# Kernel optimization log

Measured on AMD Instinct MI355X. Metric: run time of the kernel, lower is better.

## Reference

```python
import jax, jax.numpy as jnp
import numpy as np

B, T, IN, H, OUT = 64, 512, 256, 1024, 1


def _uniform(key, shape, k):
    return jax.random.uniform(key, shape, jnp.float32, -k, k)


def setup_inputs() -> dict:
    key = jax.random.key(0)
    ks = jax.random.split(key, 12)
    k = 1.0 / np.sqrt(H)
    return {
        "x": jax.random.normal(ks[0], (B, T, IN), jnp.float32),
        "W_ih0": _uniform(ks[1], (3 * H, IN), k),
        "W_hh0": _uniform(ks[2], (3 * H, H), k),
        "b_ih0": _uniform(ks[3], (3 * H,), k),
        "b_hh0": _uniform(ks[4], (3 * H,), k),
        "W_ih1": _uniform(ks[5], (3 * H, H), k),
        "W_hh1": _uniform(ks[6], (3 * H, H), k),
        "b_ih1": _uniform(ks[7], (3 * H,), k),
        "b_hh1": _uniform(ks[8], (3 * H,), k),
        "W_fc": _uniform(ks[9], (OUT, H), 1.0 / np.sqrt(H)),
        "b_fc": _uniform(ks[10], (OUT,), 1.0 / np.sqrt(H)),
    }


def _gru_layer(x, W_ih, W_hh, b_ih, b_hh):
    # x: [B, T, D_in] -> outputs [B, T, H], final hidden [B, H]
    # Precompute input projections for all timesteps (one big GEMM).
    xg = jnp.einsum('btd,gd->btg', x, W_ih) + b_ih  # [B, T, 3H]
    xg = jnp.swapaxes(xg, 0, 1)  # [T, B, 3H]

    def step(h, xg_t):
        hg = h @ W_hh.T + b_hh  # [B, 3H]
        xr, xz, xn = jnp.split(xg_t, 3, axis=-1)
        hr, hz, hn = jnp.split(hg, 3, axis=-1)
        r = jax.nn.sigmoid(xr + hr)
        z = jax.nn.sigmoid(xz + hz)
        n = jnp.tanh(xn + r * hn)
        h_new = (1.0 - z) * n + z * h
        return h_new, h_new

    h0 = jnp.zeros((x.shape[0], W_hh.shape[1]), x.dtype)
    h_final, ys = jax.lax.scan(step, h0, xg)
    return jnp.swapaxes(ys, 0, 1), h_final


def reference(x, W_ih0, W_hh0, b_ih0, b_hh0, W_ih1, W_hh1, b_ih1, b_hh1, W_fc, b_fc):
    # Inference mode: dropout (between GRU layers and before fc) is identity.
    y0, _ = _gru_layer(x, W_ih0, W_hh0, b_ih0, b_hh0)
    _, h_last = _gru_layer(y0, W_ih1, W_hh1, b_ih1, b_hh1)
    return h_last @ W_fc.T + b_fc  # [B, OUT]
```

## Files before the change

### kernel.cpp

```cpp
#include <hip/hip_runtime.h>
#include <hip/hip_bf16.h>
#include <stdint.h>


constexpr int TSEQ = 512;
constexpr int NB   = 64;
constexpr int HD   = 1024;
constexpr int IND  = 256;
constexpr int NWG  = 256;
constexpr int FS   = 16;
constexpr int PL   = NB * HD;

typedef float f32x4  __attribute__((ext_vector_type(4)));
typedef short short8 __attribute__((ext_vector_type(8)));

__device__ __forceinline__ float bf2f(unsigned u) {
    return __builtin_bit_cast(float, u << 16);
}
__device__ __forceinline__ unsigned short f2bf(float f) {
    unsigned u = __builtin_bit_cast(unsigned, f);
    u += 0x7fffu + ((u >> 16) & 1u);
    return (unsigned short)(u >> 16);
}
__device__ __forceinline__ float sigm(float x) { return 1.0f / (1.0f + __expf(-x)); }
__device__ __forceinline__ float tanh_fast(float x) { return 1.0f - 2.0f / (1.0f + __expf(2.0f * x)); }

__device__ __forceinline__ void cstore16(unsigned short* p, unsigned short v) {
    __hip_atomic_store(p, v, __ATOMIC_RELAXED, __HIP_MEMORY_SCOPE_AGENT);
}
__device__ __forceinline__ unsigned short cload16(const unsigned short* p) {
    return __hip_atomic_load(p, __ATOMIC_RELAXED, __HIP_MEMORY_SCOPE_AGENT);
}
__device__ __forceinline__ void cstoref(float* p, float v) {
    __hip_atomic_store(p, v, __ATOMIC_RELAXED, __HIP_MEMORY_SCOPE_AGENT);
}
__device__ __forceinline__ float cloadf(const float* p) {
    return __hip_atomic_load(p, __ATOMIC_RELAXED, __HIP_MEMORY_SCOPE_AGENT);
}

#define MFMA(a, b, c) __builtin_amdgcn_mfma_f32_16x16x32_bf16((a), (b), (c), 0, 0, 0)

#define LDA16(dst, base, imm) \
    asm volatile("global_load_dwordx4 %0, %1, off offset:%2 sc0 sc1" \
                 : "=v"(dst) : "v"(base), "i"(imm))
#define LDX16(dst, base, imm) \
    asm volatile("global_load_dwordx4 %0, %1, off offset:%2" \
                 : "=v"(dst) : "v"(base), "i"(imm))
#define VWAIT(n) do { asm volatile("s_waitcnt vmcnt(" #n ")" ::: "memory"); \
                      __builtin_amdgcn_sched_barrier(0); } while (0)

__global__ void convert_w(const float* __restrict__ src, unsigned short* __restrict__ dst, int n) {
    int i = blockIdx.x * blockDim.x + threadIdx.x;
    int stride = gridDim.x * blockDim.x;
    for (; i < n; i += stride) dst[i] = f2bf(src[i]);
}

__global__ __launch_bounds__(256, 1) void gru_main(
    const float* __restrict__ x,
    const unsigned short* __restrict__ wih0,
    const unsigned short* __restrict__ whh0,
    const unsigned short* __restrict__ wih1,
    const unsigned short* __restrict__ whh1,
    const float* __restrict__ bih0, const float* __restrict__ bhh0,
    const float* __restrict__ bih1, const float* __restrict__ bhh1,
    const float* __restrict__ wfc,  const float* __restrict__ bfc,
    unsigned short* __restrict__ h0hi, unsigned short* __restrict__ h0lo,
    unsigned short* __restrict__ h1hi, unsigned short* __restrict__ h1lo,
    float* __restrict__ pbuf, int* __restrict__ pflag, int* __restrict__ arrive,
    float* __restrict__ out)
{
    const int wg    = blockIdx.x;
    const int layer = wg >> 7;
    const int kh    = (wg >> 6) & 1;
    const int cc    = wg & 63;
    const int pair  = (layer << 6) | cc;
    const int jb    = cc << 4;
    const int tid   = threadIdx.x;
    const int wid   = tid >> 6;
    const int lane  = tid & 63;
    const int l15   = lane & 15;
    const int kg8   = (lane >> 4) << 3;
    const int arow  = (wid << 4) + l15;
    const int kb    = kh << 9;
    const int kbx   = kh << 7;

    const unsigned short* Whh = layer ? whh1 : whh0;
    const unsigned short* Wih = layer ? wih1 : wih0;
    const float* bih = layer ? bih1 : bih0;
    const float* bhh = layer ? bhh1 : bhh0;
    unsigned short* hhi = layer ? h1hi : h0hi;
    unsigned short* hlo = layer ? h1lo : h0lo;

    const int jg = jb + l15;
    const int KW = layer ? HD : IND;
    const int kbi = layer ? kb : kbx;
    const unsigned short* bWR = Whh + (size_t)jg          * HD + kb + kg8;
    const unsigned short* bWZ = Whh + (size_t)(HD   + jg) * HD + kb + kg8;
    const unsigned short* bWN = Whh + (size_t)(2*HD + jg) * HD + kb + kg8;
    const unsigned short* bIR = Wih + (size_t)jg          * KW + kbi + kg8;
    const unsigned short* bIZ = Wih + (size_t)(HD   + jg) * KW + kbi + kg8;
    const unsigned short* bIN = Wih + (size_t)(2*HD + jg) * KW + kbi + kg8;

    const float bias_r  = bih[jg]        + bhh[jg];
    const float bias_z  = bih[HD + jg]   + bhh[HD + jg];
    const float bias_nx = bih[2*HD + jg];
    const float bias_nh = bhh[2*HD + jg];

    __shared__ unsigned short wlds[96 * 512];
    __shared__ float red[256];

    if (wid == 0) {
        if (layer == 0) {
            const unsigned short* gh[3] = {bWR, bWZ, bWN};
            for (int s = 0; s < 3; ++s)
                for (int b = 0; b < 16; ++b)
                    *(short8*)(wlds + (s * 16 + b) * 512 + lane * 8) =
                        *(const short8*)(gh[s] + b * 32);
            const unsigned short* gi[3] = {bIR, bIZ, bIN};
            for (int s = 0; s < 3; ++s)
                for (int b = 0; b < 4; ++b)
                    *(short8*)(wlds + (48 + s * 4 + b) * 512 + lane * 8) =
                        *(const short8*)(gi[s] + b * 32);
        } else {
            const unsigned short* g6[6] = {bWR, bWZ, bWN, bIR, bIZ, bIN};
            for (int s = 0; s < 6; ++s)
                for (int b = 0; b < 16; ++b)
                    *(short8*)(wlds + (s * 16 + b) * 512 + lane * 8) =
                        *(const short8*)(g6[s] + b * 32);
        }
    }
    __syncthreads();

#define LW(blk) (*(const short8*)(wlds + (blk) * 512 + lane * 8))

    float* pb = pbuf + (size_t)pair * (16 * 256) + (wid << 6) + lane;
    float hold[4] = {0.f, 0.f, 0.f, 0.f};

    for (int iter = 0; iter <= TSEQ; ++iter) {
        const bool active = layer ? (iter >= 1) : (iter < TSEQ);
        if (active) {
            const int t     = layer ? (iter - 1) : iter;
            const int rs    = (t + 1) & 1;
            const int wslot = t & 1;
            const unsigned short* hrhi = hhi + rs * PL;
            const unsigned short* hrlo = hlo + rs * PL;
            const unsigned short* bAh = hrhi + (size_t)arow * HD + kb + kg8;
            const unsigned short* bAl = hrlo + (size_t)arow * HD + kb + kg8;

            f32x4 ar  = {0.f, 0.f, 0.f, 0.f};
            f32x4 az  = {0.f, 0.f, 0.f, 0.f};
            f32x4 ahn = {0.f, 0.f, 0.f, 0.f};
            f32x4 axn = {0.f, 0.f, 0.f, 0.f};

            if (layer == 0) {
                const float* px = x + ((size_t)arow * TSEQ + t) * IND + kbx + kg8;
                short8 Ah[5], Al[5], Wa[3], Wb[3];
#define L0A(c) do { LDA16(Ah[(c)%5], bAh, (c)*64); LDA16(Al[(c)%5], bAl, (c)*64); } while (0)
#define L0X(c) do { LDX16(Ah[(c)%5], px, ((c)-16)*128); LDX16(Al[(c)%5], px, ((c)-16)*128+16); } while (0)
#define WPRE0(c, WB) do { \
    if ((c) < 16) { WB[0] = LW(c); WB[1] = LW(16 + (c)); WB[2] = LW(32 + (c)); } \
    else { WB[0] = LW(48 + (c) - 16); WB[1] = LW(52 + (c) - 16); WB[2] = LW(56 + (c) - 16); } } while (0)
#define MR0(c, WB) do { \
    ar  = MFMA(Ah[(c)%5], WB[0], ar);  ar  = MFMA(Al[(c)%5], WB[0], ar);  \
    az  = MFMA(Ah[(c)%5], WB[1], az);  az  = MFMA(Al[(c)%5], WB[1], az);  \
    ahn = MFMA(Ah[(c)%5], WB[2], ahn); ahn = MFMA(Al[(c)%5], WB[2], ahn); } while (0)
#define MX0(c, WB) do { \
    float4 xa = __builtin_bit_cast(float4, Ah[(c)%5]); \
    float4 xc = __builtin_bit_cast(float4, Al[(c)%5]); \
    short8 af; \
    af[0] = (short)f2bf(xa.x); af[1] = (short)f2bf(xa.y); \
    af[2] = (short)f2bf(xa.z); af[3] = (short)f2bf(xa.w); \
    af[4] = (short)f2bf(xc.x); af[5] = (short)f2bf(xc.y); \
    af[6] = (short)f2bf(xc.z); af[7] = (short)f2bf(xc.w); \
    ar  = MFMA(af, WB[0], ar); \
    az  = MFMA(af, WB[1], az); \
    axn = MFMA(af, WB[2], axn); } while (0)
                WPRE0(0, Wa);
                L0A(0); L0A(1); L0A(2); L0A(3);
                WPRE0(1,  Wb); L0A(4);  VWAIT(8); MR0(0,  Wa);
                WPRE0(2,  Wa); L0A(5);  VWAIT(8); MR0(1,  Wb);
                WPRE0(3,  Wb); L0A(6);  VWAIT(8); MR0(2,  Wa);
                WPRE0(4,  Wa); L0A(7);  VWAIT(8); MR0(3,  Wb);
                WPRE0(5,  Wb); L0A(8);  VWAIT(8); MR0(4,  Wa);
                WPRE0(6,  Wa); L0A(9);  VWAIT(8); MR0(5,  Wb);
                WPRE0(7,  Wb); L0A(10); VWAIT(8); MR0(6,  Wa);
                WPRE0(8,  Wa); L0A(11); VWAIT(8); MR0(7,  Wb);
                WPRE0(9,  Wb); L0A(12); VWAIT(8); MR0(8,  Wa);
                WPRE0(10, Wa); L0A(13); VWAIT(8); MR0(9,  Wb);
                WPRE0(11, Wb); L0A(14); VWAIT(8); MR0(10, Wa);
                WPRE0(12, Wa); L0A(15); VWAIT(8); MR0(11, Wb);
                WPRE0(13, Wb); L0X(16); VWAIT(8); MR0(12, Wa);
                WPRE0(14, Wa); L0X(17); VWAIT(8); MR0(13, Wb);
                WPRE0(15, Wb); L0X(18); VWAIT(8); MR0(14, Wa);
                WPRE0(16, Wa); L0X(19); VWAIT(8); MR0(15, Wb);
                WPRE0(17, Wb); VWAIT(6); MX0(16, Wa);
                WPRE0(18, Wa); VWAIT(4); MX0(17, Wb);
                WPRE0(19, Wb); VWAIT(2); MX0(18, Wa);
                               VWAIT(0); MX0(19, Wb);
            } else {
                const unsigned short* bAy = h0hi + (size_t)wslot * PL
                                                 + (size_t)arow * HD + kb + kg8;
                short8 Ah[5], Al[5], Ay[5], Wa[6], Wb[6];
#define L1A(c) do { LDA16(Ah[(c)%5], bAh, (c)*64); LDA16(Al[(c)%5], bAl, (c)*64); \
                    LDA16(Ay[(c)%5], bAy, (c)*64); } while (0)
#define WPRE1(c, WB) do { WB[0] = LW(c); WB[1] = LW(16 + (c)); WB[2] = LW(32 + (c)); \
    WB[3] = LW(48 + (c)); WB[4] = LW(64 + (c)); WB[5] = LW(80 + (c)); } while (0)
#define MF1(c, WB) do { \
    ar  = MFMA(Ah[(c)%5], WB[0], ar);  ar  = MFMA(Al[(c)%5], WB[0], ar);  \
    ar  = MFMA(Ay[(c)%5], WB[3], ar); \
    az  = MFMA(Ah[(c)%5], WB[1], az);  az  = MFMA(Al[(c)%5], WB[1], az);  \
    az  = MFMA(Ay[(c)%5], WB[4], az); \
    ahn = MFMA(Ah[(c)%5], WB[2], ahn); ahn = MFMA(Al[(c)%5], WB[2], ahn); \
    axn = MFMA(Ay[(c)%5], WB[5], axn); } while (0)
                WPRE1(0, Wa);
                L1A(0); L1A(1); L1A(2); L1A(3);
                WPRE1(1,  Wb); L1A(4);  VWAIT(12); MF1(0,  Wa);
                WPRE1(2,  Wa); L1A(5);  VWAIT(12); MF1(1,  Wb);
                WPRE1(3,  Wb); L1A(6);  VWAIT(12); MF1(2,  Wa);
                WPRE1(4,  Wa); L1A(7);  VWAIT(12); MF1(3,  Wb);
                WPRE1(5,  Wb); L1A(8);  VWAIT(12); MF1(4,  Wa);
                WPRE1(6,  Wa); L1A(9);  VWAIT(12); MF1(5,  Wb);
                WPRE1(7,  Wb); L1A(10); VWAIT(12); MF1(6,  Wa);
                WPRE1(8,  Wa); L1A(11); VWAIT(12); MF1(7,  Wb);
                WPRE1(9,  Wb); L1A(12); VWAIT(12); MF1(8,  Wa);
                WPRE1(10, Wa); L1A(13); VWAIT(12); MF1(9,  Wb);
                WPRE1(11, Wb); L1A(14); VWAIT(12); MF1(10, Wa);
                WPRE1(12, Wa); L1A(15); VWAIT(12); MF1(11, Wb);
                WPRE1(13, Wb); VWAIT(9); MF1(12, Wa);
                WPRE1(14, Wa); VWAIT(6); MF1(13, Wb);
                WPRE1(15, Wb); VWAIT(3); MF1(14, Wa);
                               VWAIT(0); MF1(15, Wb);
            }

            int* fp = pflag + ((size_t)iter * 128 + pair) * FS;
            if (kh) {
                #pragma unroll
                for (int e = 0; e < 4; ++e) {
                    cstoref(pb + (0 * 4 + e) * 256, ar[e]);
                    cstoref(pb + (1 * 4 + e) * 256, az[e]);
                    cstoref(pb + (2 * 4 + e) * 256, ahn[e]);
                    cstoref(pb + (3 * 4 + e) * 256, axn[e]);
                }
                asm volatile("s_waitcnt vmcnt(0)" ::: "memory");
                __hip_atomic_store(fp, 1, __ATOMIC_RELAXED, __HIP_MEMORY_SCOPE_AGENT);
            } else {
                if (tid == 0) {
                    int spins = 0;
                    while (__hip_atomic_load(fp, __ATOMIC_RELAXED,
                                             __HIP_MEMORY_SCOPE_AGENT) < 1) {
                        __builtin_amdgcn_s_sleep(1);
                        if (++spins > (1 << 20)) break;
                    }
                }
                __syncthreads();
                unsigned short* hwhi = hhi + wslot * PL;
                unsigned short* hwlo = hlo + wslot * PL;
                #pragma unroll
                for (int e = 0; e < 4; ++e) {
                    const float arr = ar[e]  + cloadf(pb + (0 * 4 + e) * 256);
                    const float azz = az[e]  + cloadf(pb + (1 * 4 + e) * 256);
                    const float ahh = ahn[e] + cloadf(pb + (2 * 4 + e) * 256);
                    const float axx = axn[e] + cloadf(pb + (3 * 4 + e) * 256);
                    const int bat = (wid << 4) + ((lane >> 4) << 2) + e;
                    const size_t idx = (size_t)bat * HD + jg;
                    float r = sigm(arr + bias_r);
                    float z = sigm(azz + bias_z);
                    float n = tanh_fast(axx + bias_nx + r * (ahh + bias_nh));
                    float hnew = (1.0f - z) * n + z * hold[e];
                    hold[e] = hnew;
                    unsigned short hi_ = f2bf(hnew);
                    cstore16(hwhi + idx, hi_);
                    cstore16(hwlo + idx, f2bf(hnew - bf2f((unsigned)hi_)));
                }
            }
        }

        asm volatile("s_waitcnt vmcnt(0)" ::: "memory");
        __syncthreads();
        if (tid == 0) {
            atomicAdd(&arrive[(size_t)iter * FS], 1);
            int spins = 0;
            while (__hip_atomic_load(&arrive[(size_t)iter * FS],
                                     __ATOMIC_RELAXED, __HIP_MEMORY_SCOPE_AGENT) < NWG) {
                __builtin_amdgcn_s_sleep(1);
                if (++spins > (1 << 20)) break;
            }
        }
        __syncthreads();
    }

    if (wg == 0) {
        const int fslot = (TSEQ - 1) & 1;
        const unsigned short* hf_hi = h1hi + (size_t)fslot * PL;
        const unsigned short* hf_lo = h1lo + (size_t)fslot * PL;
        const int bat  = tid & 63;
        const int part = tid >> 6;
        const int k0   = part * (HD / 4);
        float s = 0.0f;
        for (int k = 0; k < HD / 4; ++k) {
            size_t idx = (size_t)bat * HD + k0 + k;
            s += (bf2f((unsigned)cload16(hf_hi + idx)) +
                  bf2f((unsigned)cload16(hf_lo + idx))) * wfc[k0 + k];
        }
        red[tid] = s;
        __syncthreads();
        if (tid < 64)
            out[tid] = red[tid] + red[tid + 64] + red[tid + 128] + red[tid + 192] + bfc[0];
    }
}

extern "C" void kernel_launch(void* const* d_in, const int* in_sizes, int n_in,
                              void* d_out, int out_size, void* d_ws, size_t ws_size,
                              hipStream_t stream) {
    const float* x    = (const float*)d_in[0];
    const float* Wih0 = (const float*)d_in[1];
    const float* Whh0 = (const float*)d_in[2];
    const float* bih0 = (const float*)d_in[3];
    const float* bhh0 = (const float*)d_in[4];
    const float* Wih1 = (const float*)d_in[5];
    const float* Whh1 = (const float*)d_in[6];
    const float* bih1 = (const float*)d_in[7];
    const float* bhh1 = (const float*)d_in[8];
    const float* Wfc  = (const float*)d_in[9];
    const float* bfc  = (const float*)d_in[10];
    float* out = (float*)d_out;

    char* ws = (char*)d_ws;
    size_t off = 0;
    int* arrive = (int*)(ws + off);               off += (size_t)(TSEQ + 1) * FS * 4;
    int* pflag  = (int*)(ws + off);               off += (size_t)(TSEQ + 1) * 128 * FS * 4;
    unsigned short* h0hi = (unsigned short*)(ws + off); off += (size_t)2 * PL * 2;
    unsigned short* h0lo = (unsigned short*)(ws + off); off += (size_t)2 * PL * 2;
    unsigned short* h1hi = (unsigned short*)(ws + off); off += (size_t)2 * PL * 2;
    unsigned short* h1lo = (unsigned short*)(ws + off); off += (size_t)2 * PL * 2;
    size_t zero_bytes = off;
    float* pbuf = (float*)(ws + off);             off += (size_t)128 * 16 * 256 * 4;
    unsigned short* wih0b = (unsigned short*)(ws + off); off += (size_t)3 * HD * IND * 2;
    unsigned short* whh0b = (unsigned short*)(ws + off); off += (size_t)3 * HD * HD * 2;
    unsigned short* wih1b = (unsigned short*)(ws + off); off += (size_t)3 * HD * HD * 2;
    unsigned short* whh1b = (unsigned short*)(ws + off); off += (size_t)3 * HD * HD * 2;
    if (off > ws_size) return;

    hipMemsetAsync(d_ws, 0, zero_bytes, stream);
    hipMemsetAsync(d_out, 0, (size_t)out_size * sizeof(float), stream);

    convert_w<<<512, 256, 0, stream>>>(Wih0, wih0b, 3 * HD * IND);
    convert_w<<<512, 256, 0, stream>>>(Whh0, whh0b, 3 * HD * HD);
    convert_w<<<512, 256, 0, stream>>>(Wih1, wih1b, 3 * HD * HD);
    convert_w<<<512, 256, 0, stream>>>(Whh1, whh1b, 3 * HD * HD);

    gru_main<<<NWG, 256, 0, stream>>>(x, wih0b, whh0b, wih1b, whh1b,
                                      bih0, bhh0, bih1, bhh1, Wfc, bfc,
                                      h0hi, h0lo, h1hi, h1lo,
                                      pbuf, pflag, arrive, out);
}
```

Baseline: 8.661 ms.

## Merge K-split workgroup pairs into one 512-thread block with LDS reduction

Previously two workgroups split each output tile's K range and exchanged partial sums through global memory with a per-pair flag spin. Now one 512-thread workgroup covers both K halves in separate waves and reduces through shared memory with __syncthreads. Each workgroup now handles 8 hidden columns (duplicated in the 16-wide MFMA N dimension) across 128 WGs per layer, which halves useful MFMA utilization. It removes the global partial-sum round trip and flag polling from the per-step critical path.

Result: no change. 8.586 ms (-0.9%).

```diff
diff --git a/kernel.cpp b/kernel.cpp
--- a/kernel.cpp
+++ b/kernel.cpp
@@ -29,12 +29,6 @@
     __hip_atomic_store(p, v, __ATOMIC_RELAXED, __HIP_MEMORY_SCOPE_AGENT);
 }
 __device__ __forceinline__ unsigned short cload16(const unsigned short* p) {
-    return __hip_atomic_load(p, __ATOMIC_RELAXED, __HIP_MEMORY_SCOPE_AGENT);
-}
-__device__ __forceinline__ void cstoref(float* p, float v) {
-    __hip_atomic_store(p, v, __ATOMIC_RELAXED, __HIP_MEMORY_SCOPE_AGENT);
-}
-__device__ __forceinline__ float cloadf(const float* p) {
     return __hip_atomic_load(p, __ATOMIC_RELAXED, __HIP_MEMORY_SCOPE_AGENT);
 }
 
@@ -55,7 +49,7 @@
     for (; i < n; i += stride) dst[i] = f2bf(src[i]);
 }
 
-__global__ __launch_bounds__(256, 1) void gru_main(
+__global__ __launch_bounds__(512, 2) void gru_main(
     const float* __restrict__ x,
     const unsigned short* __restrict__ wih0,
     const unsigned short* __restrict__ whh0,
@@ -66,22 +60,24 @@
     const float* __restrict__ wfc,  const float* __restrict__ bfc,
     unsigned short* __restrict__ h0hi, unsigned short* __restrict__ h0lo,
     unsigned short* __restrict__ h1hi, unsigned short* __restrict__ h1lo,
-    float* __restrict__ pbuf, int* __restrict__ pflag, int* __restrict__ arrive,
+    int* __restrict__ arrive,
     float* __restrict__ out)
 {
     const int wg    = blockIdx.x;
     const int layer = wg >> 7;
-    const int kh    = (wg >> 6) & 1;
-    const int cc    = wg & 63;
-    const int pair  = (layer << 6) | cc;
-    const int jb    = cc << 4;
+    const int cc    = wg & 127;
+    const int jb8   = cc << 3;
     const int tid   = threadIdx.x;
     const int wid   = tid >> 6;
+    const int kh    = wid >> 2;
+    const int mw    = wid & 3;
     const int lane  = tid & 63;
     const int l15   = lane & 15;
+    const int c8    = l15 & 7;
     const int kg8   = (lane >> 4) << 3;
-    const int arow  = (wid << 4) + l15;
+    const int arow  = (mw << 4) + l15;
     const int kb    = kh << 9;
+    const int ckb   = kh << 4;
     const int kbx   = kh << 7;
 
     const unsigned short* Whh = layer ? whh1 : whh0;
@@ -91,49 +87,65 @@
     unsigned short* hhi = layer ? h1hi : h0hi;
     unsigned short* hlo = layer ? h1lo : h0lo;
 
-    const int jg = jb + l15;
-    const int KW = layer ? HD : IND;
-    const int kbi = layer ? kb : kbx;
-    const unsigned short* bWR = Whh + (size_t)jg          * HD + kb + kg8;
-    const unsigned short* bWZ = Whh + (size_t)(HD   + jg) * HD + kb + kg8;
-    const unsigned short* bWN = Whh + (size_t)(2*HD + jg) * HD + kb + kg8;
-    const unsigned short* bIR = Wih + (size_t)jg          * KW + kbi + kg8;
-    const unsigned short* bIZ = Wih + (size_t)(HD   + jg) * KW + kbi + kg8;
-    const unsigned short* bIN = Wih + (size_t)(2*HD + jg) * KW + kbi + kg8;
+    const int jg = jb8 + c8;
 
     const float bias_r  = bih[jg]        + bhh[jg];
     const float bias_z  = bih[HD + jg]   + bhh[HD + jg];
     const float bias_nx = bih[2*HD + jg];
     const float bias_nh = bhh[2*HD + jg];
 
-    __shared__ unsigned short wlds[96 * 512];
+    __shared__ unsigned short wlds[192 * 256];
+    __shared__ float part[16 * 4 * 64];
     __shared__ float red[256];
 
-    if (wid == 0) {
-        if (layer == 0) {
-            const unsigned short* gh[3] = {bWR, bWZ, bWN};
-            for (int s = 0; s < 3; ++s)
-                for (int b = 0; b < 16; ++b)
-                    *(short8*)(wlds + (s * 16 + b) * 512 + lane * 8) =
-                        *(const short8*)(gh[s] + b * 32);
-            const unsigned short* gi[3] = {bIR, bIZ, bIN};
-            for (int s = 0; s < 3; ++s)
-                for (int b = 0; b < 4; ++b)
-                    *(short8*)(wlds + (48 + s * 4 + b) * 512 + lane * 8) =
-                        *(const short8*)(gi[s] + b * 32);
-        } else {
-            const unsigned short* g6[6] = {bWR, bWZ, bWN, bIR, bIZ, bIN};
-            for (int s = 0; s < 6; ++s)
-                for (int b = 0; b < 16; ++b)
-                    *(short8*)(wlds + (s * 16 + b) * 512 + lane * 8) =
-                        *(const short8*)(g6[s] + b * 32);
+    if (layer == 1) {
+        #pragma unroll
+        for (int i = 0; i < 12; ++i) {
+            int f = tid + i * 512;
+            int s   = f >> 10;
+            int rem = f & 1023;
+            int ck  = rem >> 5;
+            int hi  = (rem >> 3) & 3;
+            int c   = rem & 7;
+            const unsigned short* src = (s < 3 ? Whh : Wih)
+                + (size_t)((s % 3) * HD + jb8 + c) * HD + ck * 32 + hi * 8;
+            *(short8*)(wlds + (s * 32 + ck) * 256 + hi * 64 + c * 8) =
+                *(const short8*)src;
+        }
+    } else {
+        #pragma unroll
+        for (int i = 0; i < 6; ++i) {
+            int f = tid + i * 512;
+            int s   = f >> 10;
+            int rem = f & 1023;
+            int ck  = rem >> 5;
+            int hi  = (rem >> 3) & 3;
+            int c   = rem & 7;
+            const unsigned short* src = Whh
+                + (size_t)(s * HD + jb8 + c) * HD + ck * 32 + hi * 8;
+            *(short8*)(wlds + (s * 32 + ck) * 256 + hi * 64 + c * 8) =
+                *(const short8*)src;
+        }
+        for (int i = 0; i < 2; ++i) {
+            int f = tid + i * 512;
+            if (f < 768) {
+                int s   = f >> 8;
+                int rem = f & 255;
+                int ck  = rem >> 5;
+                int hi  = (rem >> 3) & 3;
+                int c   = rem & 7;
+                const unsigned short* src = Wih
+                    + (size_t)(s * HD + jb8 + c) * IND + ck * 32 + hi * 8;
+                *(short8*)(wlds + (96 + s * 8 + ck) * 256 + hi * 64 + c * 8) =
+                    *(const short8*)src;
+            }
         }
     }
     __syncthreads();
 
-#define LW(blk) (*(const short8*)(wlds + (blk) * 512 + lane * 8))
-
-    float* pb = pbuf + (size_t)pair * (16 * 256) + (wid << 6) + lane;
+    const int lws = (lane >> 4) * 64 + c8 * 8;
+#define LW(blk) (*(const short8*)(wlds + (blk) * 256 + lws))
+
     float hold[4] = {0.f, 0.f, 0.f, 0.f};
 
     for (int iter = 0; iter <= TSEQ; ++iter) {
@@ -157,9 +169,11 @@
                 short8 Ah[5], Al[5], Wa[3], Wb[3];
 #define L0A(c) do { LDA16(Ah[(c)%5], bAh, (c)*64); LDA16(Al[(c)%5], bAl, (c)*64); } while (0)
 #define L0X(c) do { LDX16(Ah[(c)%5], px, ((c)-16)*128); LDX16(Al[(c)%5], px, ((c)-16)*128+16); } while (0)
-#define WPRE0(c, WB) do { \
-    if ((c) < 16) { WB[0] = LW(c); WB[1] = LW(16 + (c)); WB[2] = LW(32 + (c)); } \
-    else { WB[0] = LW(48 + (c) - 16); WB[1] = LW(52 + (c) - 16); WB[2] = LW(56 + (c) - 16); } } while (0)
+#define WR0(c, WB) do { WB[0] = LW(ckb + (c)); WB[1] = LW(32 + ckb + (c)); \
+                        WB[2] = LW(64 + ckb + (c)); } while (0)
+#define WX0(c, WB) do { int xck = (ckb >> 2) + (c) - 16; \
+                        WB[0] = LW(96 + xck); WB[1] = LW(104 + xck); \
+                        WB[2] = LW(112 + xck); } while (0)
 #define MR0(c, WB) do { \
     ar  = MFMA(Ah[(c)%5], WB[0], ar);  ar  = MFMA(Al[(c)%5], WB[0], ar);  \
     az  = MFMA(Ah[(c)%5], WB[1], az);  az  = MFMA(Al[(c)%5], WB[1], az);  \
@@ -175,36 +189,37 @@
     ar  = MFMA(af, WB[0], ar); \
     az  = MFMA(af, WB[1], az); \
     axn = MFMA(af, WB[2], axn); } while (0)
-                WPRE0(0, Wa);
+                WR0(0, Wa);
                 L0A(0); L0A(1); L0A(2); L0A(3);
-                WPRE0(1,  Wb); L0A(4);  VWAIT(8); MR0(0,  Wa);
-                WPRE0(2,  Wa); L0A(5);  VWAIT(8); MR0(1,  Wb);
-                WPRE0(3,  Wb); L0A(6);  VWAIT(8); MR0(2,  Wa);
-                WPRE0(4,  Wa); L0A(7);  VWAIT(8); MR0(3,  Wb);
-                WPRE0(5,  Wb); L0A(8);  VWAIT(8); MR0(4,  Wa);
-                WPRE0(6,  Wa); L0A(9);  VWAIT(8); MR0(5,  Wb);
-                WPRE0(7,  Wb); L0A(10); VWAIT(8); MR0(6,  Wa);
-                WPRE0(8,  Wa); L0A(11); VWAIT(8); MR0(7,  Wb);
-                WPRE0(9,  Wb); L0A(12); VWAIT(8); MR0(8,  Wa);
-                WPRE0(10, Wa); L0A(13); VWAIT(8); MR0(9,  Wb);
-                WPRE0(11, Wb); L0A(14); VWAIT(8); MR0(10, Wa);
-                WPRE0(12, Wa); L0A(15); VWAIT(8); MR0(11, Wb);
-                WPRE0(13, Wb); L0X(16); VWAIT(8); MR0(12, Wa);
-                WPRE0(14, Wa); L0X(17); VWAIT(8); MR0(13, Wb);
-                WPRE0(15, Wb); L0X(18); VWAIT(8); MR0(14, Wa);
-                WPRE0(16, Wa); L0X(19); VWAIT(8); MR0(15, Wb);
-                WPRE0(17, Wb); VWAIT(6); MX0(16, Wa);
-                WPRE0(18, Wa); VWAIT(4); MX0(17, Wb);
-                WPRE0(19, Wb); VWAIT(2); MX0(18, Wa);
-                               VWAIT(0); MX0(19, Wb);
+                WR0(1,  Wb); L0A(4);  VWAIT(8); MR0(0,  Wa);
+                WR0(2,  Wa); L0A(5);  VWAIT(8); MR0(1,  Wb);
+                WR0(3,  Wb); L0A(6);  VWAIT(8); MR0(2,  Wa);
+                WR0(4,  Wa); L0A(7);  VWAIT(8); MR0(3,  Wb);
+                WR0(5,  Wb); L0A(8);  VWAIT(8); MR0(4,  Wa);
+                WR0(6,  Wa); L0A(9);  VWAIT(8); MR0(5,  Wb);
+                WR0(7,  Wb); L0A(10); VWAIT(8); MR0(6,  Wa);
+                WR0(8,  Wa); L0A(11); VWAIT(8); MR0(7,  Wb);
+                WR0(9,  Wb); L0A(12); VWAIT(8); MR0(8,  Wa);
+                WR0(10, Wa); L0A(13); VWAIT(8); MR0(9,  Wb);
+                WR0(11, Wb); L0A(14); VWAIT(8); MR0(10, Wa);
+                WR0(12, Wa); L0A(15); VWAIT(8); MR0(11, Wb);
+                WR0(13, Wb); L0X(16); VWAIT(8); MR0(12, Wa);
+                WR0(14, Wa); L0X(17); VWAIT(8); MR0(13, Wb);
+                WR0(15, Wb); L0X(18); VWAIT(8); MR0(14, Wa);
+                WX0(16, Wa); L0X(19); VWAIT(8); MR0(15, Wb);
+                WX0(17, Wb); VWAIT(6); MX0(16, Wa);
+                WX0(18, Wa); VWAIT(4); MX0(17, Wb);
+                WX0(19, Wb); VWAIT(2); MX0(18, Wa);
+                             VWAIT(0); MX0(19, Wb);
             } else {
                 const unsigned short* bAy = h0hi + (size_t)wslot * PL
                                                  + (size_t)arow * HD + kb + kg8;
                 short8 Ah[5], Al[5], Ay[5], Wa[6], Wb[6];
 #define L1A(c) do { LDA16(Ah[(c)%5], bAh, (c)*64); LDA16(Al[(c)%5], bAl, (c)*64); \
                     LDA16(Ay[(c)%5], bAy, (c)*64); } while (0)
-#define WPRE1(c, WB) do { WB[0] = LW(c); WB[1] = LW(16 + (c)); WB[2] = LW(32 + (c)); \
-    WB[3] = LW(48 + (c)); WB[4] = LW(64 + (c)); WB[5] = LW(80 + (c)); } while (0)
+#define WR1(c, WB) do { WB[0] = LW(ckb + (c)); WB[1] = LW(32 + ckb + (c)); \
+    WB[2] = LW(64 + ckb + (c)); WB[3] = LW(96 + ckb + (c)); \
+    WB[4] = LW(128 + ckb + (c)); WB[5] = LW(160 + ckb + (c)); } while (0)
 #define MF1(c, WB) do { \
     ar  = MFMA(Ah[(c)%5], WB[0], ar);  ar  = MFMA(Al[(c)%5], WB[0], ar);  \
     ar  = MFMA(Ay[(c)%5], WB[3], ar); \
@@ -212,65 +227,57 @@
     az  = MFMA(Ay[(c)%5], WB[4], az); \
     ahn = MFMA(Ah[(c)%5], WB[2], ahn); ahn = MFMA(Al[(c)%5], WB[2], ahn); \
     axn = MFMA(Ay[(c)%5], WB[5], axn); } while (0)
-                WPRE1(0, Wa);
+                WR1(0, Wa);
                 L1A(0); L1A(1); L1A(2); L1A(3);
-                WPRE1(1,  Wb); L1A(4);  VWAIT(12); MF1(0,  Wa);
-                WPRE1(2,  Wa); L1A(5);  VWAIT(12); MF1(1,  Wb);
-                WPRE1(3,  Wb); L1A(6);  VWAIT(12); MF1(2,  Wa);
-                WPRE1(4,  Wa); L1A(7);  VWAIT(12); MF1(3,  Wb);
-                WPRE1(5,  Wb); L1A(8);  VWAIT(12); MF1(4,  Wa);
-                WPRE1(6,  Wa); L1A(9);  VWAIT(12); MF1(5,  Wb);
-                WPRE1(7,  Wb); L1A(10); VWAIT(12); MF1(6,  Wa);
-                WPRE1(8,  Wa); L1A(11); VWAIT(12); MF1(7,  Wb);
-                WPRE1(9,  Wb); L1A(12); VWAIT(12); MF1(8,  Wa);
-                WPRE1(10, Wa); L1A(13); VWAIT(12); MF1(9,  Wb);
-                WPRE1(11, Wb); L1A(14); VWAIT(12); MF1(10, Wa);
-                WPRE1(12, Wa); L1A(15); VWAIT(12); MF1(11, Wb);
-                WPRE1(13, Wb); VWAIT(9); MF1(12, Wa);
-                WPRE1(14, Wa); VWAIT(6); MF1(13, Wb);
-                WPRE1(15, Wb); VWAIT(3); MF1(14, Wa);
-                               VWAIT(0); MF1(15, Wb);
-            }
-
-            int* fp = pflag + ((size_t)iter * 128 + pair) * FS;
+                WR1(1,  Wb); L1A(4);  VWAIT(12); MF1(0,  Wa);
+                WR1(2,  Wa); L1A(5);  VWAIT(12); MF1(1,  Wb);
+                WR1(3,  Wb); L1A(6);  VWAIT(12); MF1(2,  Wa);
+                WR1(4,  Wa); L1A(7);  VWAIT(12); MF1(3,  Wb);
+                WR1(5,  Wb); L1A(8);  VWAIT(12); MF1(4,  Wa);
+                WR1(6,  Wa); L1A(9);  VWAIT(12); MF1(5,  Wb);
+                WR1(7,  Wb); L1A(10); VWAIT(12); MF1(6,  Wa);
+                WR1(8,  Wa); L1A(11); VWAIT(12); MF1(7,  Wb);
+                WR1(9,  Wb); L1A(12); VWAIT(12); MF1(8,  Wa);
+                WR1(10, Wa); L1A(13); VWAIT(12); MF1(9,  Wb);
+                WR1(11, Wb); L1A(14); VWAIT(12); MF1(10, Wa);
+                WR1(12, Wa); L1A(15); VWAIT(12); MF1(11, Wb);
+                WR1(13, Wb); VWAIT(9); MF1(12, Wa);
+                WR1(14, Wa); VWAIT(6); MF1(13, Wb);
+                WR1(15, Wb); VWAIT(3); MF1(14, Wa);
+                             VWAIT(0); MF1(15, Wb);
+            }
+
             if (kh) {
                 #pragma unroll
                 for (int e = 0; e < 4; ++e) {
-                    cstoref(pb + (0 * 4 + e) * 256, ar[e]);
-                    cstoref(pb + (1 * 4 + e) * 256, az[e]);
-                    cstoref(pb + (2 * 4 + e) * 256, ahn[e]);
-                    cstoref(pb + (3 * 4 + e) * 256, axn[e]);
+                    part[((0*4 + e) * 4 + mw) * 64 + lane] = ar[e];
+                    part[((1*4 + e) * 4 + mw) * 64 + lane] = az[e];
+                    part[((2*4 + e) * 4 + mw) * 64 + lane] = ahn[e];
+                    part[((3*4 + e) * 4 + mw) * 64 + lane] = axn[e];
                 }
-                asm volatile("s_waitcnt vmcnt(0)" ::: "memory");
-                __hip_atomic_store(fp, 1, __ATOMIC_RELAXED, __HIP_MEMORY_SCOPE_AGENT);
-            } else {
-                if (tid == 0) {
-                    int spins = 0;
-                    while (__hip_atomic_load(fp, __ATOMIC_RELAXED,
-                                             __HIP_MEMORY_SCOPE_AGENT) < 1) {
-                        __builtin_amdgcn_s_sleep(1);
-                        if (++spins > (1 << 20)) break;
-                    }
-                }
-                __syncthreads();
+            }
+            __syncthreads();
+            if (!kh) {
                 unsigned short* hwhi = hhi + wslot * PL;
                 unsigned short* hwlo = hlo + wslot * PL;
                 #pragma unroll
                 for (int e = 0; e < 4; ++e) {
-                    const float arr = ar[e]  + cloadf(pb + (0 * 4 + e) * 256);
-                    const float azz = az[e]  + cloadf(pb + (1 * 4 + e) * 256);
-                    const float ahh = ahn[e] + cloadf(pb + (2 * 4 + e) * 256);
-                    const float axx = axn[e] + cloadf(pb + (3 * 4 + e) * 256);
-                    const int bat = (wid << 4) + ((lane >> 4) << 2) + e;
+                    const float arr = ar[e]  + part[((0*4 + e) * 4 + mw) * 64 + lane];
+                    const float azz = az[e]  + part[((1*4 + e) * 4 + mw) * 64 + lane];
+                    const float ahh = ahn[e] + part[((2*4 + e) * 4 + mw) * 64 + lane];
+                    const float axx = axn[e] + part[((3*4 + e) * 4 + mw) * 64 + lane];
+                    const int bat = (mw << 4) + ((lane >> 4) << 2) + e;
                     const size_t idx = (size_t)bat * HD + jg;
                     float r = sigm(arr + bias_r);
                     float z = sigm(azz + bias_z);
                     float n = tanh_fast(axx + bias_nx + r * (ahh + bias_nh));
                     float hnew = (1.0f - z) * n + z * hold[e];
                     hold[e] = hnew;
-                    unsigned short hi_ = f2bf(hnew);
-                    cstore16(hwhi + idx, hi_);
-                    cstore16(hwlo + idx, f2bf(hnew - bf2f((unsigned)hi_)));
+                    if (l15 < 8) {
+                        unsigned short hi_ = f2bf(hnew);
+                        cstore16(hwhi + idx, hi_);
+                        cstore16(hwlo + idx, f2bf(hnew - bf2f((unsigned)hi_)));
+                    }
                 }
             }
         }
@@ -293,16 +300,18 @@
         const int fslot = (TSEQ - 1) & 1;
         const unsigned short* hf_hi = h1hi + (size_t)fslot * PL;
         const unsigned short* hf_lo = h1lo + (size_t)fslot * PL;
-        const int bat  = tid & 63;
-        const int part = tid >> 6;
-        const int k0   = part * (HD / 4);
-        float s = 0.0f;
-        for (int k = 0; k < HD / 4; ++k) {
-            size_t idx = (size_t)bat * HD + k0 + k;
-            s += (bf2f((unsigned)cload16(hf_hi + idx)) +
-                  bf2f((unsigned)cload16(hf_lo + idx))) * wfc[k0 + k];
-        }
-        red[tid] = s;
+        if (tid < 256) {
+            const int bat  = tid & 63;
+            const int pidx = tid >> 6;
+            const int k0   = pidx * (HD / 4);
+            float s = 0.0f;
+            for (int k = 0; k < HD / 4; ++k) {
+                size_t idx = (size_t)bat * HD + k0 + k;
+                s += (bf2f((unsigned)cload16(hf_hi + idx)) +
+                      bf2f((unsigned)cload16(hf_lo + idx))) * wfc[k0 + k];
+            }
+            red[tid] = s;
+        }
         __syncthreads();
         if (tid < 64)
             out[tid] = red[tid] + red[tid + 64] + red[tid + 128] + red[tid + 192] + bfc[0];
@@ -328,13 +337,11 @@
     char* ws = (char*)d_ws;
     size_t off = 0;
     int* arrive = (int*)(ws + off);               off += (size_t)(TSEQ + 1) * FS * 4;
-    int* pflag  = (int*)(ws + off);               off += (size_t)(TSEQ + 1) * 128 * FS * 4;
     unsigned short* h0hi = (unsigned short*)(ws + off); off += (size_t)2 * PL * 2;
     unsigned short* h0lo = (unsigned short*)(ws + off); off += (size_t)2 * PL * 2;
     unsigned short* h1hi = (unsigned short*)(ws + off); off += (size_t)2 * PL * 2;
     unsigned short* h1lo = (unsigned short*)(ws + off); off += (size_t)2 * PL * 2;
     size_t zero_bytes = off;
-    float* pbuf = (float*)(ws + off);             off += (size_t)128 * 16 * 256 * 4;
     unsigned short* wih0b = (unsigned short*)(ws + off); off += (size_t)3 * HD * IND * 2;
     unsigned short* whh0b = (unsigned short*)(ws + off); off += (size_t)3 * HD * HD * 2;
     unsigned short* wih1b = (unsigned short*)(ws + off); off += (size_t)3 * HD * HD * 2;
@@ -349,8 +356,7 @@
     convert_w<<<512, 256, 0, stream>>>(Wih1, wih1b, 3 * HD * HD);
     convert_w<<<512, 256, 0, stream>>>(Whh1, whh1b, 3 * HD * HD);
 
-    gru_main<<<NWG, 256, 0, stream>>>(x, wih0b, whh0b, wih1b, whh1b,
+    gru_main<<<NWG, 512, 0, stream>>>(x, wih0b, whh0b, wih1b, whh1b,
                                       bih0, bhh0, bih1, bhh1, Wfc, bfc,
-                                      h0hi, h0lo, h1hi, h1lo,
-                                      pbuf, pflag, arrive, out);
-}
+                                      h0hi, h0lo, h1hi, h1lo, arrive, out);
+}
```
